# Kernel optimization log

Measured on AMD Instinct MI355X. Metric: run time of the kernel, lower is better.

Reference implementation:

```python
import jax, jax.numpy as jnp
import numpy as np

D_MODEL = 512
NUM_HEADS = 8
D_HEAD = 64
BATCH = 2
SEQ = 2048
NEG_BIG = 1.0e10


def setup_inputs() -> dict:
    key = jax.random.key(0)
    k1, k2, k3, k4, k5 = jax.random.split(key, 5)
    scale = D_MODEL ** -0.5
    return {
        "x": jax.random.normal(k1, (BATCH, SEQ, D_MODEL), dtype=jnp.float32),
        "W_Q": jax.random.normal(k2, (NUM_HEADS, D_HEAD, D_MODEL), dtype=jnp.float32) * scale,
        "W_K": jax.random.normal(k3, (NUM_HEADS, D_HEAD, D_MODEL), dtype=jnp.float32) * scale,
        "W_V": jax.random.normal(k4, (NUM_HEADS, D_HEAD, D_MODEL), dtype=jnp.float32) * scale,
        "W_O": jax.random.normal(k5, (D_MODEL, D_HEAD * NUM_HEADS), dtype=jnp.float32) * scale,
    }


def reference(x, W_Q, W_K, W_V, W_O):
    b, n, d = x.shape
    # q,k,v: [b, heads, pos, d_head]
    q = jnp.einsum('ihd,bpd->biph', W_Q, x)
    k = jnp.einsum('ihd,bpd->biph', W_K, x)
    v = jnp.einsum('ihd,bpd->biph', W_V, x)
    # scores: [b, heads, q_pos, k_pos]
    scores = jnp.einsum('biph,biqh->biqp', k, q)
    tril = jnp.tril(jnp.ones((n, n), dtype=scores.dtype))   # keep p <= q
    triu = jnp.triu(jnp.ones((n, n), dtype=scores.dtype))   # buffer 'mask'
    # Faithful to source: tril(scores) - 1e10 * (1 - triu)
    masked = scores * tril - NEG_BIG * (1.0 - triu)
    attn = jax.nn.softmax(masked / (D_HEAD ** 0.5), axis=-1)
    z = jnp.einsum('biph,biqp->biqh', v, attn)               # [b, i, q, h]
    z_flat = jnp.transpose(z, (0, 2, 1, 3)).reshape(b, n, -1)  # [b, q, i*h]
    out = jnp.einsum('df,bqf->bqd', W_O, z_flat)
    return out
```

## Files before the change

kernel.cpp:

```cpp
#include <hip/hip_runtime.h>
#include <stdint.h>

#define BATCH 2
#define SEQ 2048
#define DM 512
#define NH 8
#define DH 64
#define MROWS (BATCH * SEQ)
#define NCHUNK 64
#define CHUNK (SEQ / NCHUNK)

typedef __attribute__((ext_vector_type(8))) short bf16x8;
typedef __attribute__((ext_vector_type(4))) float f32x4;

__device__ __forceinline__ unsigned short f2bf(float f) {
    union { float f; uint32_t u; } x; x.f = f;
    uint32_t r = x.u + 0x7fffu + ((x.u >> 16) & 1u);
    return (unsigned short)(r >> 16);
}
__device__ __forceinline__ float bf2f(unsigned short s) {
    union { uint32_t u; float f; } x; x.u = ((uint32_t)s) << 16;
    return x.f;
}

__device__ __forceinline__ void gl_lds16(const void* g, void* l) {
    __builtin_amdgcn_global_load_lds(
        (const __attribute__((address_space(1))) void*)(uintptr_t)g,
        (__attribute__((address_space(3))) void*)(uint32_t)(uintptr_t)l,
        16, 0, 0);
}

__global__ void cvt_all(const float4* __restrict__ x,
                        const float4* __restrict__ Wq, const float4* __restrict__ Wk,
                        const float4* __restrict__ Wv, const float4* __restrict__ Wo,
                        ushort4* __restrict__ xb, ushort4* __restrict__ wb) {
    int i = blockIdx.x * blockDim.x + threadIdx.x;
    float4 v; ushort4* dst; int off;
    if (i < 524288) {
        v = x[i]; dst = xb; off = i;
    } else {
        int j = i - 524288;
        if (j < 131072) {
            int head = j >> 14, rp = (j >> 7) & 127, colq = j & 127;
            v = (rp < 64) ? Wq[head * 8192 + rp * 128 + colq]
                          : Wk[head * 8192 + (rp - 64) * 128 + colq];
        } else if (j < 196608) {
            v = Wv[j - 131072];
        } else {
            v = Wo[j - 196608];
        }
        dst = wb; off = j;
    }
    ushort4 o; o.x = f2bf(v.x); o.y = f2bf(v.y); o.z = f2bf(v.z); o.w = f2bf(v.w);
    dst[off] = o;
}

__global__ __launch_bounds__(256) void proj(
    const unsigned short* __restrict__ xb, const unsigned short* __restrict__ wb,
    float* __restrict__ cA, float* __restrict__ cW,
    unsigned short* __restrict__ V, float* __restrict__ csum)
{
    __shared__ __align__(16) unsigned short S[2 * 256 * 64];
    const int t = threadIdx.x, lane = t & 63, wave = t >> 6;
    const int lr = lane >> 3;
    const int csrc = ((lane & 7) ^ lr) * 8;
    const int l15 = lane & 15, q = lane >> 4;
    const int bid = blockIdx.x;
    const int wm = wave * 32;

    if (bid < 256) {
        constexpr int TE = 256 * 64;
        const int head = bid & 7, m0 = (bid >> 3) * 128;
        const unsigned short* Bw = wb + head * 65536;
        const unsigned short* gb[8];
#pragma unroll
        for (int r = 0; r < 8; r++) {
            int s = r * 4 + wave, g = s * 8 + lr;
            gb[r] = (g < 128) ? xb + (size_t)(m0 + g) * 512 + csrc
                              : Bw + (size_t)(g - 128) * 512 + csrc;
        }
        f32x4 acc[2][8];
#pragma unroll
        for (int i = 0; i < 2; i++)
#pragma unroll
            for (int j = 0; j < 8; j++) { f32x4 z = {0.f,0.f,0.f,0.f}; acc[i][j] = z; }

        auto stage = [&](unsigned short* Sb, int k0) {
#pragma unroll
            for (int r = 0; r < 8; r++)
                gl_lds16(gb[r] + k0, Sb + (r * 4 + wave) * 512);
        };
        auto compute = [&](const unsigned short* Sb) {
#pragma unroll
            for (int h = 0; h < 2; h++) {
                bf16x8 af[2], bfr[8];
#pragma unroll
                for (int i = 0; i < 2; i++) {
                    int R = wm + i * 16 + l15;
                    af[i] = *(const bf16x8*)(Sb + R * 64 + (((q + 4 * h) ^ (R & 7)) * 8));
                }
#pragma unroll
                for (int j = 0; j < 8; j++) {
                    int R = 128 + j * 16 + l15;
                    bfr[j] = *(const bf16x8*)(Sb + R * 64 + (((q + 4 * h) ^ (R & 7)) * 8));
                }
#pragma unroll
                for (int i = 0; i < 2; i++)
#pragma unroll
                    for (int j = 0; j < 8; j++)
                        acc[i][j] = __builtin_amdgcn_mfma_f32_16x16x32_bf16(af[i], bfr[j], acc[i][j], 0, 0, 0);
            }
        };

        stage(S, 0);
        asm volatile("s_waitcnt vmcnt(0)" ::: "memory");
        __builtin_amdgcn_s_barrier();
        int cur = 0;
        for (int k0 = 64; k0 < 512; k0 += 64) {
            stage(S + (cur ^ 1) * TE, k0);
            compute(S + cur * TE);
            asm volatile("s_waitcnt vmcnt(0)" ::: "memory");
            __builtin_amdgcn_s_barrier();
            cur ^= 1;
        }
        compute(S + cur * TE);

#pragma unroll
        for (int i = 0; i < 2; i++)
#pragma unroll
            for (int r = 0; r < 4; r++) {
                float d = 0.f;
#pragma unroll
                for (int j = 0; j < 4; j++) d += acc[i][j][r] * acc[i][j + 4][r];
                d += __shfl_xor(d, 1); d += __shfl_xor(d, 2);
                d += __shfl_xor(d, 4); d += __shfl_xor(d, 8);
                if (l15 == 0) {
                    int row = m0 + wm + i * 16 + (lane >> 4) * 4 + r;
                    int p = row & (SEQ - 1);
                    float dd = d * 0.125f;
                    float M = fmaxf(dd, 0.f);
                    float a = expf(dd - M), e0 = expf(-M);
                    float Z = a + (float)(SEQ - 1 - p) * e0;
                    cA[row * NH + head] = a / Z;
                    cW[row * NH + head] = e0 / Z;
                }
            }
    } else {
        constexpr int TE = 192 * 64;
        const int b2 = bid - 256;
        const int head = b2 & 7, m0 = (b2 >> 3) * 128, n0 = head * 64;
        const unsigned short* Bv = wb + 524288 + (size_t)n0 * 512;
        const unsigned short* gb[6];
#pragma unroll
        for (int r = 0; r < 6; r++) {
            int s = r * 4 + wave, g = s * 8 + lr;
            gb[r] = (g < 128) ? xb + (size_t)(m0 + g) * 512 + csrc
                              : Bv + (size_t)(g - 128) * 512 + csrc;
        }
        f32x4 acc[2][4];
#pragma unroll
        for (int i = 0; i < 2; i++)
#pragma unroll
            for (int j = 0; j < 4; j++) { f32x4 z = {0.f,0.f,0.f,0.f}; acc[i][j] = z; }

        auto stage = [&](unsigned short* Sb, int k0) {
#pragma unroll
            for (int r = 0; r < 6; r++)
                gl_lds16(gb[r] + k0, Sb + (r * 4 + wave) * 512);
        };
        auto compute = [&](const unsigned short* Sb) {
#pragma unroll
            for (int h = 0; h < 2; h++) {
                bf16x8 af[2], bfr[4];
#pragma unroll
                for (int i = 0; i < 2; i++) {
                    int R = wm + i * 16 + l15;
                    af[i] = *(const bf16x8*)(Sb + R * 64 + (((q + 4 * h) ^ (R & 7)) * 8));
                }
#pragma unroll
                for (int j = 0; j < 4; j++) {
                    int R = 128 + j * 16 + l15;
                    bfr[j] = *(const bf16x8*)(Sb + R * 64 + (((q + 4 * h) ^ (R & 7)) * 8));
                }
#pragma unroll
                for (int i = 0; i < 2; i++)
#pragma unroll
                    for (int j = 0; j < 4; j++)
                        acc[i][j] = __builtin_amdgcn_mfma_f32_16x16x32_bf16(af[i], bfr[j], acc[i][j], 0, 0, 0);
            }
        };

        stage(S, 0);
        asm volatile("s_waitcnt vmcnt(0)" ::: "memory");
        __builtin_amdgcn_s_barrier();
        int cur = 0;
        for (int k0 = 64; k0 < 512; k0 += 64) {
            stage(S + (cur ^ 1) * TE, k0);
            compute(S + cur * TE);
            asm volatile("s_waitcnt vmcnt(0)" ::: "memory");
            __builtin_amdgcn_s_barrier();
            cur ^= 1;
        }
        compute(S + cur * TE);

        const int crow = m0 + wm + (lane >> 4) * 4;
#pragma unroll
        for (int i = 0; i < 2; i++)
#pragma unroll
            for (int j = 0; j < 4; j++)
#pragma unroll
                for (int r = 0; r < 4; r++)
                    V[(size_t)(crow + i * 16 + r) * DM + n0 + j * 16 + l15] = f2bf(acc[i][j][r]);
        float s[4];
#pragma unroll
        for (int j = 0; j < 4; j++) {
            s[j] = 0.f;
#pragma unroll
            for (int i = 0; i < 2; i++)
#pragma unroll
                for (int r = 0; r < 4; r++) s[j] += acc[i][j][r];
            s[j] += __shfl_xor(s[j], 16);
            s[j] += __shfl_xor(s[j], 32);
        }
        if (lane < 16) {
            int bi = (m0 >> 11) * NH + head;
            int chunk = ((m0 & (SEQ - 1)) >> 5) + wave;
#pragma unroll
            for (int j = 0; j < 4; j++)
                csum[(bi * NCHUNK + chunk) * 64 + j * 16 + lane] = s[j];
        }
    }
}

__global__ __launch_bounds__(256) void zbuild(
    const unsigned short* __restrict__ V, const float* __restrict__ csum,
    const float* __restrict__ cA, const float* __restrict__ cW,
    unsigned short* __restrict__ Zb) {
    int ci = blockIdx.x * 4 + (threadIdx.x >> 6);
    int h = threadIdx.x & 63;
    int c = ci & (NCHUNK - 1), bi = ci >> 6;
    int i = bi & 7, b = bi >> 3;
    float r = 0.f;
    for (int cc = c + 1; cc < NCHUNK; cc++) r += csum[((bi << 6) + cc) * 64 + h];
    for (int j = CHUNK - 1; j >= 0; j--) {
        int p = c * CHUNK + j;
        size_t row = (size_t)(b * SEQ + p);
        float v = bf2f(V[row * DM + i * DH + h]);
        float a = cA[row * NH + i], w = cW[row * NH + i];
        Zb[row * DM + i * DH + h] = f2bf(fmaf(a, v, w * r));
        r += v;
    }
}

template<int TM, int TN, int WM, int WN>
__global__ __launch_bounds__(256) void gemm_bt(
    const unsigned short* __restrict__ A, const unsigned short* __restrict__ B,
    float* __restrict__ C, int M, int N, int K)
{
    constexpr int ROWS = TM + TN;
    constexpr int SPW = ROWS / 32;
    constexpr int MI = WM / 16, NJ = WN / 16;
    constexpr int WAVES_N = TN / WN;
    constexpr int TE = ROWS * 64;
    __shared__ __align__(16) unsigned short S[2 * TE];
    const int t = threadIdx.x, lane = t & 63, wave = t >> 6;
    const int wm = (wave / WAVES_N) * WM, wn = (wave % WAVES_N) * WN;
    const int m0 = blockIdx.x * TM, n0 = blockIdx.y * TN;
    const int lr = lane >> 3;
    const int csrc = ((lane & 7) ^ lr) * 8;
    const int l15 = lane & 15, q = lane >> 4;

    const unsigned short* gb[SPW];
#pragma unroll
    for (int r = 0; r < SPW; r++) {
        int s = r * 4 + wave, g = s * 8 + lr;
        gb[r] = (g < TM) ? A + (size_t)(m0 + g) * K + csrc
                         : B + (size_t)(n0 + g - TM) * K + csrc;
    }

    f32x4 acc[MI][NJ];
#pragma unroll
    for (int i = 0; i < MI; i++)
#pragma unroll
        for (int j = 0; j < NJ; j++) { f32x4 z = {0.f,0.f,0.f,0.f}; acc[i][j] = z; }

    auto stage = [&](unsigned short* Sb, int k0) {
#pragma unroll
        for (int r = 0; r < SPW; r++)
            gl_lds16(gb[r] + k0, Sb + (r * 4 + wave) * 512);
    };
    auto compute = [&](const unsigned short* Sb) {
#pragma unroll
        for (int h = 0; h < 2; h++) {
            bf16x8 af[MI], bfr[NJ];
#pragma unroll
            for (int i = 0; i < MI; i++) {
                int R = wm + i * 16 + l15;
                af[i] = *(const bf16x8*)(Sb + R * 64 + (((q + 4 * h) ^ (R & 7)) * 8));
            }
#pragma unroll
            for (int j = 0; j < NJ; j++) {
                int R = TM + wn + j * 16 + l15;
                bfr[j] = *(const bf16x8*)(Sb + R * 64 + (((q + 4 * h) ^ (R & 7)) * 8));
            }
#pragma unroll
            for (int i = 0; i < MI; i++)
#pragma unroll
                for (int j = 0; j < NJ; j++)
                    acc[i][j] = __builtin_amdgcn_mfma_f32_16x16x32_bf16(af[i], bfr[j], acc[i][j], 0, 0, 0);
        }
    };

    stage(S, 0);
    asm volatile("s_waitcnt vmcnt(0)" ::: "memory");
    __builtin_amdgcn_s_barrier();
    int cur = 0;
    for (int k0 = 64; k0 < K; k0 += 64) {
        stage(S + (cur ^ 1) * TE, k0);
        compute(S + cur * TE);
        asm volatile("s_waitcnt vmcnt(0)" ::: "memory");
        __builtin_amdgcn_s_barrier();
        cur ^= 1;
    }
    compute(S + cur * TE);

    const int crow = m0 + wm + (lane >> 4) * 4;
    const int ccol = n0 + wn + (lane & 15);
#pragma unroll
    for (int i = 0; i < MI; i++)
#pragma unroll
        for (int j = 0; j < NJ; j++)
#pragma unroll
            for (int r = 0; r < 4; r++)
                C[(size_t)(crow + i * 16 + r) * N + ccol + j * 16] = acc[i][j][r];
}

extern "C" void kernel_launch(void* const* d_in, const int* in_sizes, int n_in,
                              void* d_out, int out_size, void* d_ws, size_t ws_size,
                              hipStream_t stream) {
    const float* x  = (const float*)d_in[0];
    const float* Wq = (const float*)d_in[1];
    const float* Wk = (const float*)d_in[2];
    const float* Wv = (const float*)d_in[3];
    const float* Wo = (const float*)d_in[4];
    float* out = (float*)d_out;
    char* ws = (char*)d_ws;

    unsigned short* xb = (unsigned short*)(ws);
    unsigned short* wb = (unsigned short*)(ws + 4194304);
    unsigned short* V  = (unsigned short*)(ws + 6291456);
    float* cA = (float*)(ws + 10485760);
    float* cW = (float*)(ws + 10616832);
    float* cs = (float*)(ws + 10747904);
    unsigned short* Zb = (unsigned short*)(ws + 11010048);

    cvt_all<<<3072, 256, 0, stream>>>((const float4*)x, (const float4*)Wq,
                                      (const float4*)Wk, (const float4*)Wv,
                                      (const float4*)Wo, (ushort4*)xb, (ushort4*)wb);
    proj<<<512, 256, 0, stream>>>(xb, wb, cA, cW, V, cs);
    zbuild<<<256, 256, 0, stream>>>(V, cs, cA, cW, Zb);
    gemm_bt<64, 64, 32, 32><<<dim3(64, 8, 1), 256, 0, stream>>>(
        Zb, wb + 786432, out, MROWS, DM, DM);
}
```

Measured before the change: 103.6 us.

## Use 4-stage LDS pipeline with 32-wide K tiles in projection and GEMM kernels

Replaces the double-buffered 64-wide K loop with a four-buffer ring of 32-wide K tiles, keeping three loads in flight via partial vmcnt waits so a wave no longer drains all loads before each barrier. LDS offsets are precomputed once with a new XOR swizzle for the 32-column layout, and MFMA bursts are wrapped in s_setprio. It also adds unroll pragmas to the scan kernel loops. The price is twice as many barriers per K, and the hardcoded vmcnt counts tie correctness to the exact number of loads issued per stage.

```diff
diff --git a/kernel.cpp b/kernel.cpp
--- a/kernel.cpp
+++ b/kernel.cpp
@@ -60,70 +60,77 @@
     float* __restrict__ cA, float* __restrict__ cW,
     unsigned short* __restrict__ V, float* __restrict__ csum)
 {
-    __shared__ __align__(16) unsigned short S[2 * 256 * 64];
+    __shared__ __align__(16) unsigned short S[4 * 256 * 32];
     const int t = threadIdx.x, lane = t & 63, wave = t >> 6;
-    const int lr = lane >> 3;
-    const int csrc = ((lane & 7) ^ lr) * 8;
+    const int lr2 = lane >> 2;
+    const int csrc = ((lane & 3) ^ ((lane >> 3) & 3)) * 8;
     const int l15 = lane & 15, q = lane >> 4;
     const int bid = blockIdx.x;
     const int wm = wave * 32;
 
     if (bid < 256) {
-        constexpr int TE = 256 * 64;
+        constexpr int TE = 256 * 32;
         const int head = bid & 7, m0 = (bid >> 3) * 128;
         const unsigned short* Bw = wb + head * 65536;
-        const unsigned short* gb[8];
-#pragma unroll
-        for (int r = 0; r < 8; r++) {
-            int s = r * 4 + wave, g = s * 8 + lr;
+        const unsigned short* gb[4];
+#pragma unroll
+        for (int r = 0; r < 4; r++) {
+            int g = (r * 4 + wave) * 16 + lr2;
             gb[r] = (g < 128) ? xb + (size_t)(m0 + g) * 512 + csrc
                               : Bw + (size_t)(g - 128) * 512 + csrc;
         }
+        int aoff[2], boff[8];
+#pragma unroll
+        for (int i = 0; i < 2; i++) {
+            int R = wm + i * 16 + l15;
+            aoff[i] = R * 32 + ((q ^ ((R >> 1) & 3)) * 8);
+        }
+#pragma unroll
+        for (int j = 0; j < 8; j++) {
+            int R = 128 + j * 16 + l15;
+            boff[j] = R * 32 + ((q ^ ((R >> 1) & 3)) * 8);
+        }
         f32x4 acc[2][8];
 #pragma unroll
         for (int i = 0; i < 2; i++)
 #pragma unroll
             for (int j = 0; j < 8; j++) { f32x4 z = {0.f,0.f,0.f,0.f}; acc[i][j] = z; }
 
-        auto stage = [&](unsigned short* Sb, int k0) {
-#pragma unroll
-            for (int r = 0; r < 8; r++)
-                gl_lds16(gb[r] + k0, Sb + (r * 4 + wave) * 512);
+        auto stage = [&](int buf, int tt) {
+            const int k0 = tt * 32;
+#pragma unroll
+            for (int r = 0; r < 4; r++)
+                gl_lds16(gb[r] + k0, S + buf * TE + (r * 4 + wave) * 512);
         };
-        auto compute = [&](const unsigned short* Sb) {
-#pragma unroll
-            for (int h = 0; h < 2; h++) {
-                bf16x8 af[2], bfr[8];
-#pragma unroll
-                for (int i = 0; i < 2; i++) {
-                    int R = wm + i * 16 + l15;
-                    af[i] = *(const bf16x8*)(Sb + R * 64 + (((q + 4 * h) ^ (R & 7)) * 8));
-                }
-#pragma unroll
-                for (int j = 0; j < 8; j++) {
-                    int R = 128 + j * 16 + l15;
-                    bfr[j] = *(const bf16x8*)(Sb + R * 64 + (((q + 4 * h) ^ (R & 7)) * 8));
-                }
-#pragma unroll
-                for (int i = 0; i < 2; i++)
-#pragma unroll
-                    for (int j = 0; j < 8; j++)
-                        acc[i][j] = __builtin_amdgcn_mfma_f32_16x16x32_bf16(af[i], bfr[j], acc[i][j], 0, 0, 0);
-            }
+        auto compute = [&](int buf) {
+            const unsigned short* Sb = S + buf * TE;
+            bf16x8 af[2], bfr[8];
+#pragma unroll
+            for (int i = 0; i < 2; i++) af[i] = *(const bf16x8*)(Sb + aoff[i]);
+#pragma unroll
+            for (int j = 0; j < 8; j++) bfr[j] = *(const bf16x8*)(Sb + boff[j]);
+            __builtin_amdgcn_s_setprio(1);
+#pragma unroll
+            for (int i = 0; i < 2; i++)
+#pragma unroll
+                for (int j = 0; j < 8; j++)
+                    acc[i][j] = __builtin_amdgcn_mfma_f32_16x16x32_bf16(af[i], bfr[j], acc[i][j], 0, 0, 0);
+            __builtin_amdgcn_s_setprio(0);
         };
 
-        stage(S, 0);
+        stage(0, 0); stage(1, 1); stage(2, 2);
+        for (int tt = 0; tt < 14; ++tt) {
+            asm volatile("s_waitcnt vmcnt(8)" ::: "memory");
+            __builtin_amdgcn_s_barrier();
+            compute(tt & 3);
+            if (tt <= 12) stage((tt + 3) & 3, tt + 3);
+        }
+        asm volatile("s_waitcnt vmcnt(4)" ::: "memory");
+        __builtin_amdgcn_s_barrier();
+        compute(2);
         asm volatile("s_waitcnt vmcnt(0)" ::: "memory");
         __builtin_amdgcn_s_barrier();
-        int cur = 0;
-        for (int k0 = 64; k0 < 512; k0 += 64) {
-            stage(S + (cur ^ 1) * TE, k0);
-            compute(S + cur * TE);
-            asm volatile("s_waitcnt vmcnt(0)" ::: "memory");
-            __builtin_amdgcn_s_barrier();
-            cur ^= 1;
-        }
-        compute(S + cur * TE);
+        compute(3);
 
 #pragma unroll
         for (int i = 0; i < 2; i++)
@@ -146,62 +153,69 @@
                 }
             }
     } else {
-        constexpr int TE = 192 * 64;
+        constexpr int TE2 = 192 * 32;
         const int b2 = bid - 256;
         const int head = b2 & 7, m0 = (b2 >> 3) * 128, n0 = head * 64;
         const unsigned short* Bv = wb + 524288 + (size_t)n0 * 512;
-        const unsigned short* gb[6];
-#pragma unroll
-        for (int r = 0; r < 6; r++) {
-            int s = r * 4 + wave, g = s * 8 + lr;
+        const unsigned short* gb[3];
+#pragma unroll
+        for (int r = 0; r < 3; r++) {
+            int g = (r * 4 + wave) * 16 + lr2;
             gb[r] = (g < 128) ? xb + (size_t)(m0 + g) * 512 + csrc
                               : Bv + (size_t)(g - 128) * 512 + csrc;
         }
+        int aoff[2], boff[4];
+#pragma unroll
+        for (int i = 0; i < 2; i++) {
+            int R = wm + i * 16 + l15;
+            aoff[i] = R * 32 + ((q ^ ((R >> 1) & 3)) * 8);
+        }
+#pragma unroll
+        for (int j = 0; j < 4; j++) {
+            int R = 128 + j * 16 + l15;
+            boff[j] = R * 32 + ((q ^ ((R >> 1) & 3)) * 8);
+        }
         f32x4 acc[2][4];
 #pragma unroll
         for (int i = 0; i < 2; i++)
 #pragma unroll
             for (int j = 0; j < 4; j++) { f32x4 z = {0.f,0.f,0.f,0.f}; acc[i][j] = z; }
 
-        auto stage = [&](unsigned short* Sb, int k0) {
-#pragma unroll
-            for (int r = 0; r < 6; r++)
-                gl_lds16(gb[r] + k0, Sb + (r * 4 + wave) * 512);
+        auto stage = [&](int buf, int tt) {
+            const int k0 = tt * 32;
+#pragma unroll
+            for (int r = 0; r < 3; r++)
+                gl_lds16(gb[r] + k0, S + buf * TE2 + (r * 4 + wave) * 512);
         };
-        auto compute = [&](const unsigned short* Sb) {
-#pragma unroll
-            for (int h = 0; h < 2; h++) {
-                bf16x8 af[2], bfr[4];
-#pragma unroll
-                for (int i = 0; i < 2; i++) {
-                    int R = wm + i * 16 + l15;
-                    af[i] = *(const bf16x8*)(Sb + R * 64 + (((q + 4 * h) ^ (R & 7)) * 8));
-                }
-#pragma unroll
-                for (int j = 0; j < 4; j++) {
-                    int R = 128 + j * 16 + l15;
-                    bfr[j] = *(const bf16x8*)(Sb + R * 64 + (((q + 4 * h) ^ (R & 7)) * 8));
-                }
-#pragma unroll
-                for (int i = 0; i < 2; i++)
-#pragma unroll
-                    for (int j = 0; j < 4; j++)
-                        acc[i][j] = __builtin_amdgcn_mfma_f32_16x16x32_bf16(af[i], bfr[j], acc[i][j], 0, 0, 0);
-            }
+        auto compute = [&](int buf) {
+            const unsigned short* Sb = S + buf * TE2;
+            bf16x8 af[2], bfr[4];
+#pragma unroll
+            for (int i = 0; i < 2; i++) af[i] = *(const bf16x8*)(Sb + aoff[i]);
+#pragma unroll
+            for (int j = 0; j < 4; j++) bfr[j] = *(const bf16x8*)(Sb + boff[j]);
+            __builtin_amdgcn_s_setprio(1);
+#pragma unroll
+            for (int i = 0; i < 2; i++)
+#pragma unroll
+                for (int j = 0; j < 4; j++)
+                    acc[i][j] = __builtin_amdgcn_mfma_f32_16x16x32_bf16(af[i], bfr[j], acc[i][j], 0, 0, 0);
+            __builtin_amdgcn_s_setprio(0);
         };
 
-        stage(S, 0);
+        stage(0, 0); stage(1, 1); stage(2, 2);
+        for (int tt = 0; tt < 14; ++tt) {
+            asm volatile("s_waitcnt vmcnt(6)" ::: "memory");
+            __builtin_amdgcn_s_barrier();
+            compute(tt & 3);
+            if (tt <= 12) stage((tt + 3) & 3, tt + 3);
+        }
+        asm volatile("s_waitcnt vmcnt(3)" ::: "memory");
+        __builtin_amdgcn_s_barrier();
+        compute(2);
         asm volatile("s_waitcnt vmcnt(0)" ::: "memory");
         __builtin_amdgcn_s_barrier();
-        int cur = 0;
-        for (int k0 = 64; k0 < 512; k0 += 64) {
-            stage(S + (cur ^ 1) * TE, k0);
-            compute(S + cur * TE);
-            asm volatile("s_waitcnt vmcnt(0)" ::: "memory");
-            __builtin_amdgcn_s_barrier();
-            cur ^= 1;
-        }
-        compute(S + cur * TE);
+        compute(3);
 
         const int crow = m0 + wm + (lane >> 4) * 4;
 #pragma unroll
@@ -241,7 +255,9 @@
     int c = ci & (NCHUNK - 1), bi = ci >> 6;
     int i = bi & 7, b = bi >> 3;
     float r = 0.f;
+#pragma unroll 4
     for (int cc = c + 1; cc < NCHUNK; cc++) r += csum[((bi << 6) + cc) * 64 + h];
+#pragma unroll 4
     for (int j = CHUNK - 1; j >= 0; j--) {
         int p = c * CHUNK + j;
         size_t row = (size_t)(b * SEQ + p);
@@ -258,25 +274,36 @@
     float* __restrict__ C, int M, int N, int K)
 {
     constexpr int ROWS = TM + TN;
-    constexpr int SPW = ROWS / 32;
+    static_assert(ROWS == 128, "pipeline waits assume 128 staged rows");
     constexpr int MI = WM / 16, NJ = WN / 16;
     constexpr int WAVES_N = TN / WN;
-    constexpr int TE = ROWS * 64;
-    __shared__ __align__(16) unsigned short S[2 * TE];
+    constexpr int TE = ROWS * 32;
+    __shared__ __align__(16) unsigned short S[4 * TE];
     const int t = threadIdx.x, lane = t & 63, wave = t >> 6;
     const int wm = (wave / WAVES_N) * WM, wn = (wave % WAVES_N) * WN;
     const int m0 = blockIdx.x * TM, n0 = blockIdx.y * TN;
-    const int lr = lane >> 3;
-    const int csrc = ((lane & 7) ^ lr) * 8;
+    const int lr2 = lane >> 2;
+    const int csrc = ((lane & 3) ^ ((lane >> 3) & 3)) * 8;
     const int l15 = lane & 15, q = lane >> 4;
 
-    const unsigned short* gb[SPW];
-#pragma unroll
-    for (int r = 0; r < SPW; r++) {
-        int s = r * 4 + wave, g = s * 8 + lr;
+    const unsigned short* gb[2];
+#pragma unroll
+    for (int r = 0; r < 2; r++) {
+        int g = (r * 4 + wave) * 16 + lr2;
         gb[r] = (g < TM) ? A + (size_t)(m0 + g) * K + csrc
                          : B + (size_t)(n0 + g - TM) * K + csrc;
     }
+    int aoff[MI], boff[NJ];
+#pragma unroll
+    for (int i = 0; i < MI; i++) {
+        int R = wm + i * 16 + l15;
+        aoff[i] = R * 32 + ((q ^ ((R >> 1) & 3)) * 8);
+    }
+#pragma unroll
+    for (int j = 0; j < NJ; j++) {
+        int R = TM + wn + j * 16 + l15;
+        boff[j] = R * 32 + ((q ^ ((R >> 1) & 3)) * 8);
+    }
 
     f32x4 acc[MI][NJ];
 #pragma unroll
@@ -284,45 +311,42 @@
 #pragma unroll
         for (int j = 0; j < NJ; j++) { f32x4 z = {0.f,0.f,0.f,0.f}; acc[i][j] = z; }
 
-    auto stage = [&](unsigned short* Sb, int k0) {
-#pragma unroll
-        for (int r = 0; r < SPW; r++)
-            gl_lds16(gb[r] + k0, Sb + (r * 4 + wave) * 512);
+    auto stage = [&](int buf, int tt) {
+        const int k0 = tt * 32;
+#pragma unroll
+        for (int r = 0; r < 2; r++)
+            gl_lds16(gb[r] + k0, S + buf * TE + (r * 4 + wave) * 512);
     };
-    auto compute = [&](const unsigned short* Sb) {
-#pragma unroll
-        for (int h = 0; h < 2; h++) {
-            bf16x8 af[MI], bfr[NJ];
-#pragma unroll
-            for (int i = 0; i < MI; i++) {
-                int R = wm + i * 16 + l15;
-                af[i] = *(const bf16x8*)(Sb + R * 64 + (((q + 4 * h) ^ (R & 7)) * 8));
-            }
-#pragma unroll
-            for (int j = 0; j < NJ; j++) {
-                int R = TM + wn + j * 16 + l15;
-                bfr[j] = *(const bf16x8*)(Sb + R * 64 + (((q + 4 * h) ^ (R & 7)) * 8));
-            }
-#pragma unroll
-            for (int i = 0; i < MI; i++)
-#pragma unroll
-                for (int j = 0; j < NJ; j++)
-                    acc[i][j] = __builtin_amdgcn_mfma_f32_16x16x32_bf16(af[i], bfr[j], acc[i][j], 0, 0, 0);
-        }
+    auto compute = [&](int buf) {
+        const unsigned short* Sb = S + buf * TE;
+        bf16x8 af[MI], bfr[NJ];
+#pragma unroll
+        for (int i = 0; i < MI; i++) af[i] = *(const bf16x8*)(Sb + aoff[i]);
+#pragma unroll
+        for (int j = 0; j < NJ; j++) bfr[j] = *(const bf16x8*)(Sb + boff[j]);
+        __builtin_amdgcn_s_setprio(1);
+#pragma unroll
+        for (int i = 0; i < MI; i++)
+#pragma unroll
+            for (int j = 0; j < NJ; j++)
+                acc[i][j] = __builtin_amdgcn_mfma_f32_16x16x32_bf16(af[i], bfr[j], acc[i][j], 0, 0, 0);
+        __builtin_amdgcn_s_setprio(0);
     };
 
-    stage(S, 0);
+    const int NT = K / 32;
+    stage(0, 0); stage(1, 1); stage(2, 2);
+    for (int tt = 0; tt < NT - 2; ++tt) {
+        asm volatile("s_waitcnt vmcnt(4)" ::: "memory");
+        __builtin_amdgcn_s_barrier();
+        compute(tt & 3);
+        if (tt + 3 < NT) stage((tt + 3) & 3, tt + 3);
+    }
+    asm volatile("s_waitcnt vmcnt(2)" ::: "memory");
+    __builtin_amdgcn_s_barrier();
+    compute((NT - 2) & 3);
     asm volatile("s_waitcnt vmcnt(0)" ::: "memory");
     __builtin_amdgcn_s_barrier();
-    int cur = 0;
-    for (int k0 = 64; k0 < K; k0 += 64) {
-        stage(S + (cur ^ 1) * TE, k0);
-        compute(S + cur * TE);
-        asm volatile("s_waitcnt vmcnt(0)" ::: "memory");
-        __builtin_amdgcn_s_barrier();
-        cur ^= 1;
-    }
-    compute(S + cur * TE);
+    compute((NT - 1) & 3);
 
     const int crow = m0 + wm + (lane >> 4) * 4;
     const int ccol = n0 + wn + (lane & 15);
```

After: 101.2 us. -2.3%, faster.
